# Optimization experiments

Hardware: AMD Instinct MI355X
Metric: run time of the kernel (lower is better)

Reference implementation:

```python
import jax, jax.numpy as jnp
import numpy as np

N_NODES = 50000
N_EDGES = 1600000
IN_C = 64
OUT_C = 64
N_CLASSES = 45


def setup_inputs() -> dict:
    key = jax.random.key(0)
    ks = jax.random.split(key, 12)

    def lin(k, i, o):
        return jax.random.normal(k, (i, o), jnp.float32) / np.float32(np.sqrt(i))

    return dict(
        x=jax.random.normal(ks[0], (N_NODES, IN_C), jnp.float32),
        edge_index=jax.random.randint(ks[1], (2, N_EDGES), 0, N_NODES, dtype=jnp.int32),
        W_z=lin(ks[2], IN_C, OUT_C), b_z=jnp.zeros((OUT_C,), jnp.float32),
        Wl_z=lin(ks[3], 2 * OUT_C, OUT_C), bl_z=jnp.zeros((OUT_C,), jnp.float32),
        W_r=lin(ks[4], IN_C, OUT_C), b_r=jnp.zeros((OUT_C,), jnp.float32),
        Wl_r=lin(ks[5], 2 * OUT_C, OUT_C), bl_r=jnp.zeros((OUT_C,), jnp.float32),
        W_h=lin(ks[6], IN_C, OUT_C), b_h=jnp.zeros((OUT_C,), jnp.float32),
        Wl_h=lin(ks[7], 2 * OUT_C, OUT_C), bl_h=jnp.zeros((OUT_C,), jnp.float32),
        W_out=lin(ks[8], OUT_C, N_CLASSES), b_out=jnp.zeros((N_CLASSES,), jnp.float32),
    )


def _gcn(x, W, b, src, dst, dinv):
    # GCNConv with improved self-loops (fill value 2.0):
    # out = D^{-1/2} (A + 2I) D^{-1/2} X W + b, with deg = in_degree + 2
    xw = x @ W                                   # [N, OUT_C]
    norm = dinv[src] * dinv[dst]                 # [E]
    agg = jax.ops.segment_sum(norm[:, None] * xw[src], dst, num_segments=N_NODES)
    agg = agg + (2.0 * dinv * dinv)[:, None] * xw  # self-loop contribution
    return agg + b


def reference(x, edge_index, W_z, b_z, Wl_z, bl_z, W_r, b_r, Wl_r, bl_r,
              W_h, b_h, Wl_h, bl_h, W_out, b_out):
    src, dst = edge_index[0], edge_index[1]
    deg = jax.ops.segment_sum(jnp.ones((N_EDGES,), jnp.float32), dst,
                              num_segments=N_NODES) + 2.0
    dinv = jax.lax.rsqrt(deg)

    # TGCN cell with H0 = 0 (no prior hidden state passed)
    H = jnp.zeros((N_NODES, OUT_C), x.dtype)
    Z = jax.nn.sigmoid(
        jnp.concatenate([_gcn(x, W_z, b_z, src, dst, dinv), H], axis=1) @ Wl_z + bl_z)
    R = jax.nn.sigmoid(
        jnp.concatenate([_gcn(x, W_r, b_r, src, dst, dinv), H], axis=1) @ Wl_r + bl_r)
    H_tilde = jnp.tanh(
        jnp.concatenate([_gcn(x, W_h, b_h, src, dst, dinv), H * R], axis=1) @ Wl_h + bl_h)
    H = Z * H + (1.0 - Z) * H_tilde

    # relu + linear readout to 45 classes
    return jax.nn.relu(H) @ W_out + b_out
```

## Files before the change

### kernel.cpp

```cpp
#include <hip/hip_runtime.h>

#define N_NODES 50000
#define N_EDGES 1600000
#define NB 782
#define NBB 500
#define CHUNK 3200
#define CAP 2560
#define SCAP 3072
#define ZROW 50000
#define NTILES 3125

typedef unsigned short ushort_t;
typedef _Float16 v8h __attribute__((ext_vector_type(8)));
typedef _Float16 v4h __attribute__((ext_vector_type(4)));
typedef float f32x4_t __attribute__((ext_vector_type(4)));

__global__ __launch_bounds__(256) void k_wprep2(
    const float* __restrict__ Wz, const float* __restrict__ bz,
    const float* __restrict__ Wlz, const float* __restrict__ blz,
    const float* __restrict__ Wh, const float* __restrict__ bh,
    const float* __restrict__ Wlh, const float* __restrict__ blh,
    const float* __restrict__ Wout,
    float* __restrict__ B2f, _Float16* __restrict__ Bzh,
    _Float16* __restrict__ Bwo, int* __restrict__ gcur) {
  __shared__ float A[64 * 65];
  __shared__ float Bm[64 * 65];
  int tid = threadIdx.x, blk = blockIdx.x;
  bool zpath = blk < 4;
  if (blk == 2) {
    for (int i = tid; i < NB; i += 256) gcur[i] = 0;
  }
  const float* Wsrc = zpath ? Wz : Wh;
  const float* Lsrc = zpath ? Wlz : Wlh;
  for (int idx = tid; idx < 4096; idx += 256) {
    A[(idx >> 6) * 65 + (idx & 63)] = Wsrc[idx];
    Bm[(idx >> 6) * 65 + (idx & 63)] = Lsrc[idx];
  }
  __syncthreads();

  int lane = (tid >> 1) & 63;
  int j0 = (tid & 1) * 4;
  int ks = (tid >> 7) & 1;
  int k0 = ks * 32 + ((lane >> 4) << 3) + j0;
  int col = (blk & 3) * 16 + (lane & 15);
  float a0 = 0.f, a1 = 0.f, a2 = 0.f, a3 = 0.f;
  for (int q = 0; q < 64; ++q) {
    float bv = Bm[q * 65 + col];
    a0 = fmaf(A[k0 * 65 + q], bv, a0);
    a1 = fmaf(A[(k0 + 1) * 65 + q], bv, a1);
    a2 = fmaf(A[(k0 + 2) * 65 + q], bv, a2);
    a3 = fmaf(A[(k0 + 3) * 65 + q], bv, a3);
  }
  int tb = blk * 1024 + tid * 4;
  v4h o; o[0] = (_Float16)a0; o[1] = (_Float16)a1;
  o[2] = (_Float16)a2; o[3] = (_Float16)a3;
  *(v4h*)(Bzh + tb) = o;

  if ((blk == 0 || blk == 4) && tid < 64) {
    float v = zpath ? blz[tid] : blh[tid];
    const float* bb = zpath ? bz : bh;
    for (int q = 0; q < 64; ++q) v = fmaf(bb[q], Bm[q * 65 + tid], v);
    B2f[tid * 2 + (zpath ? 0 : 1)] = v;
  }
  if (blk == 1) {
    for (int e2 = 0; e2 < 12; ++e2) {
      int t2 = tid * 12 + e2;
      int ln = (t2 >> 3) & 63, j = t2 & 7;
      int ntile = t2 >> 10, ks2 = (t2 >> 9) & 1;
      int n = ntile * 16 + (ln & 15);
      int k = ks2 * 32 + ((ln >> 4) << 3) + j;
      Bwo[t2] = (_Float16)((n < 45) ? Wout[k * 45 + n] : 0.f);
    }
  }
}

__global__ __launch_bounds__(256) void k_bin2(
    const int* __restrict__ ei, int* __restrict__ gcur, int* __restrict__ bins) {
  __shared__ int h[NB], cur[NB], segb[NB];
  __shared__ int ebuf[CHUNK];
  __shared__ int scanT[256];
  int tid = threadIdx.x, blk = blockIdx.x;
  for (int i = tid; i < NB; i += 256) h[i] = 0;
  __syncthreads();
  int e0 = blk * CHUNK;
  const int2* d2 = (const int2*)(ei + N_EDGES + e0);
  for (int i = tid; i < CHUNK / 2; i += 256) {
    int2 d = d2[i];
    atomicAdd(&h[d.x >> 6], 1);
    atomicAdd(&h[d.y >> 6], 1);
  }
  __syncthreads();
  for (int b = tid; b < NB; b += 256) {
    int c = h[b];
    segb[b] = c ? atomicAdd(&gcur[b], c) : 0;
  }
  int vals[4], ts = 0;
  #pragma unroll
  for (int r = 0; r < 4; ++r) {
    int idx = tid * 4 + r;
    int v = (idx < NB) ? h[idx] : 0;
    vals[r] = v; ts += v;
  }
  scanT[tid] = ts;
  __syncthreads();
  for (int off = 1; off < 256; off <<= 1) {
    int u = (tid >= off) ? scanT[tid - off] : 0;
    __syncthreads();
    scanT[tid] += u;
    __syncthreads();
  }
  int ex = scanT[tid] - ts;
  #pragma unroll
  for (int r = 0; r < 4; ++r) {
    int idx = tid * 4 + r;
    if (idx < NB) cur[idx] = ex;
    ex += vals[r];
  }
  __syncthreads();
  const int2* s2 = (const int2*)(ei + e0);
  for (int i = tid; i < CHUNK / 2; i += 256) {
    int2 s = s2[i];
    int2 d = d2[i];
    int b0 = d.x >> 6, b1 = d.y >> 6;
    int p0 = atomicAdd(&cur[b0], 1);
    ebuf[p0] = s.x | ((d.x & 63) << 16) | (b0 << 22);
    int p1 = atomicAdd(&cur[b1], 1);
    ebuf[p1] = s.y | ((d.y & 63) << 16) | (b1 << 22);
  }
  __syncthreads();
  for (int i = tid; i < CHUNK; i += 256) {
    int v = ebuf[i];
    int b = (unsigned)v >> 22;
    int ex0 = cur[b] - h[b];
    bins[b * CAP + segb[b] + (i - ex0)] = v & 0x3FFFFF;
  }
}

__global__ __launch_bounds__(256, 4) void k_sort(
    const int* __restrict__ bins, const int* __restrict__ gcur,
    const float* __restrict__ x,
    ushort_t* __restrict__ srcp, int2* __restrict__ rowiv,
    float* __restrict__ dinv, _Float16* __restrict__ xp) {
  __shared__ int dg[64], lo[64], cur[64];
  __shared__ float sdin[64];
  __shared__ int Tsh;
  __shared__ ushort_t buf[3072];
  int tid = threadIdx.x, b = blockIdx.x;
  int start = b * CAP, end = start + gcur[b];
  if (tid < 64) dg[tid] = 0;
  __syncthreads();
  for (int i = start + tid; i < end; i += 256)
    atomicAdd(&dg[bins[i] >> 16], 1);
  __syncthreads();
  int pdv = 0;
  if (tid < 64) { pdv = (dg[tid] + 7) & ~7; lo[tid] = pdv; }
  __syncthreads();
  for (int off = 1; off < 64; off <<= 1) {
    int u = 0;
    if (tid < 64 && tid >= off) u = lo[tid - off];
    __syncthreads();
    if (tid < 64) lo[tid] += u;
    __syncthreads();
  }
  int ex = 0;
  if (tid < 64) {
    ex = lo[tid] - pdv;
    cur[tid] = ex;
    if (tid == 63) Tsh = lo[63];
  }
  __syncthreads();
  int T = Tsh;
  int base = b * SCAP;
  for (int i = tid; i < T; i += 256) buf[i] = (ushort_t)ZROW;
  __syncthreads();
  for (int i = start + tid; i < end; i += 256) {
    int v = bins[i];
    int dl = v >> 16;
    int p = atomicAdd(&cur[dl], 1);
    buf[p] = (ushort_t)(v & 0xFFFF);
  }
  __syncthreads();
  for (int i = tid; i < T; i += 256) srcp[base + i] = buf[i];
  if (tid < 64) {
    int v = b * 64 + tid;
    if (v < N_NODES) {
      rowiv[v] = make_int2(base + ex, pdv);
      float dv = rsqrtf((float)dg[tid] + 2.0f);
      dinv[v] = dv;
      sdin[tid] = dv;
    } else {
      sdin[tid] = 0.f;
    }
  }
  __syncthreads();
  int nb64 = b * 4096;
  for (int idx = tid; idx < 4096; idx += 256) {
    int v = b * 64 + (idx >> 6);
    if (v < N_NODES) xp[nb64 + idx] = (_Float16)(sdin[idx >> 6] * x[nb64 + idx]);
  }
  if (b == 0 && tid < 64) xp[ZROW * 64 + tid] = (_Float16)0.f;
}

__global__ __launch_bounds__(256) void k_agg(
    const ushort_t* __restrict__ srcp, const int2* __restrict__ rowiv,
    const float* __restrict__ dinv, const _Float16* __restrict__ xp,
    _Float16* __restrict__ sxg) {
  int tid = threadIdx.x;
  int lane = tid & 63;
  int grp = lane >> 4;
  int sub = lane & 15;
  int chOff = sub << 2;
  int w = blockIdx.x * 4 + (tid >> 6);
  int nw = gridDim.x * 4;
  for (int v = w; v < N_NODES; v += nw) {
    int vu = __builtin_amdgcn_readfirstlane(v);
    int2 ri = rowiv[vu];
    int beg = ri.x, pd = ri.y;
    float aA0 = 0.f, aA1 = 0.f, aA2 = 0.f, aA3 = 0.f;
    float aB0 = 0.f, aB1 = 0.f, aB2 = 0.f, aB3 = 0.f;
    float aC0 = 0.f, aC1 = 0.f, aC2 = 0.f, aC3 = 0.f;
    float aD0 = 0.f, aD1 = 0.f, aD2 = 0.f, aD3 = 0.f;
    for (int e = beg; e < beg + pd; e += 64) {
      int rem = beg + pd - e;
      int m = rem < 64 ? rem : 64;
      int sv = (lane < m) ? (int)srcp[e + lane] : ZROW;
      int t = 0;
      for (; t + 16 <= m; t += 16) {
        int sA = __builtin_amdgcn_ds_bpermute((t + grp) << 2, sv);
        int sB = __builtin_amdgcn_ds_bpermute((t + 4 + grp) << 2, sv);
        int sC = __builtin_amdgcn_ds_bpermute((t + 8 + grp) << 2, sv);
        int sD = __builtin_amdgcn_ds_bpermute((t + 12 + grp) << 2, sv);
        v4h rA = *(const v4h*)(xp + (sA << 6) + chOff);
        v4h rB = *(const v4h*)(xp + (sB << 6) + chOff);
        v4h rC = *(const v4h*)(xp + (sC << 6) + chOff);
        v4h rD = *(const v4h*)(xp + (sD << 6) + chOff);
        aA0 += (float)rA[0]; aA1 += (float)rA[1];
        aA2 += (float)rA[2]; aA3 += (float)rA[3];
        aB0 += (float)rB[0]; aB1 += (float)rB[1];
        aB2 += (float)rB[2]; aB3 += (float)rB[3];
        aC0 += (float)rC[0]; aC1 += (float)rC[1];
        aC2 += (float)rC[2]; aC3 += (float)rC[3];
        aD0 += (float)rD[0]; aD1 += (float)rD[1];
        aD2 += (float)rD[2]; aD3 += (float)rD[3];
      }
      if (t < m) {
        int sA = __builtin_amdgcn_ds_bpermute((t + grp) << 2, sv);
        int sB = __builtin_amdgcn_ds_bpermute((t + 4 + grp) << 2, sv);
        v4h rA = *(const v4h*)(xp + (sA << 6) + chOff);
        v4h rB = *(const v4h*)(xp + (sB << 6) + chOff);
        aA0 += (float)rA[0]; aA1 += (float)rA[1];
        aA2 += (float)rA[2]; aA3 += (float)rA[3];
        aB0 += (float)rB[0]; aB1 += (float)rB[1];
        aB2 += (float)rB[2]; aB3 += (float)rB[3];
      }
    }
    float a0 = (aA0 + aB0) + (aC0 + aD0);
    float a1 = (aA1 + aB1) + (aC1 + aD1);
    float a2 = (aA2 + aB2) + (aC2 + aD2);
    float a3 = (aA3 + aB3) + (aC3 + aD3);
    a0 += __shfl_xor(a0, 16); a1 += __shfl_xor(a1, 16);
    a2 += __shfl_xor(a2, 16); a3 += __shfl_xor(a3, 16);
    a0 += __shfl_xor(a0, 32); a1 += __shfl_xor(a1, 32);
    a2 += __shfl_xor(a2, 32); a3 += __shfl_xor(a3, 32);
    if (lane < 16) {
      float dv = dinv[vu];
      v4h self = *(const v4h*)(xp + (vu << 6) + chOff);
      v4h o;
      o[0] = (_Float16)(dv * a0 + 2.f * dv * (float)self[0]);
      o[1] = (_Float16)(dv * a1 + 2.f * dv * (float)self[1]);
      o[2] = (_Float16)(dv * a2 + 2.f * dv * (float)self[2]);
      o[3] = (_Float16)(dv * a3 + 2.f * dv * (float)self[3]);
      *(v4h*)(sxg + (vu << 6) + chOff) = o;
    }
  }
}

__global__ __launch_bounds__(256) void k_cell(
    const _Float16* __restrict__ sxg, const _Float16* __restrict__ Bzh,
    const _Float16* __restrict__ Bwo, const float2* __restrict__ B2,
    const float* __restrict__ bout, float* __restrict__ out) {
  __shared__ __align__(16) _Float16 tbuf[4][16][72];
  int tid = threadIdx.x;
  int lane = tid & 63, wv = tid >> 6;
  int l15 = lane & 15, quad = lane >> 4;
  int tile = blockIdx.x * 4 + wv;
  if (tile >= NTILES) return;

  v8h bzf[8][2], bwf[3][2];
  #pragma unroll
  for (int t = 0; t < 8; ++t)
    #pragma unroll
    for (int ks = 0; ks < 2; ++ks)
      bzf[t][ks] = *(const v8h*)(Bzh + (((t * 2 + ks) * 64 + lane) << 3));
  #pragma unroll
  for (int t = 0; t < 3; ++t)
    #pragma unroll
    for (int ks = 0; ks < 2; ++ks)
      bwf[t][ks] = *(const v8h*)(Bwo + (((t * 2 + ks) * 64 + lane) << 3));
  float zb[4], hb[4], ob[3];
  #pragma unroll
  for (int t = 0; t < 4; ++t) {
    float2 bb = B2[t * 16 + l15];
    zb[t] = bb.x; hb[t] = bb.y;
  }
  #pragma unroll
  for (int t = 0; t < 3; ++t) {
    int c = t * 16 + l15;
    ob[t] = (c < 45) ? bout[c] : 0.f;
  }

  const _Float16* ar = sxg + (tile * 16 + l15) * 64 + quad * 8;
  v8h a0 = *(const v8h*)ar;
  v8h a1 = *(const v8h*)(ar + 32);

  f32x4_t accz[8];
  #pragma unroll
  for (int t = 0; t < 8; ++t) {
    f32x4_t c4 = {0.f, 0.f, 0.f, 0.f};
    c4 = __builtin_amdgcn_mfma_f32_16x16x32_f16(a0, bzf[t][0], c4, 0, 0, 0);
    c4 = __builtin_amdgcn_mfma_f32_16x16x32_f16(a1, bzf[t][1], c4, 0, 0, 0);
    accz[t] = c4;
  }

  #pragma unroll
  for (int t = 0; t < 4; ++t) {
    #pragma unroll
    for (int r = 0; r < 4; ++r) {
      float zv = accz[t][r] + zb[t];
      float hv = accz[t + 4][r] + hb[t];
      float Z = 1.f / (1.f + __expf(-zv));
      float tt = fminf(15.f, fmaxf(-15.f, hv));
      float e2 = __expf(-2.f * tt);
      float Th = (1.f - e2) / (1.f + e2);
      tbuf[wv][quad * 4 + r][t * 16 + l15] = (_Float16)fmaxf((1.f - Z) * Th, 0.f);
    }
  }
  __asm__ volatile("s_waitcnt lgkmcnt(0)" ::: "memory");

  v8h p0 = *(const v8h*)&tbuf[wv][l15][quad * 8];
  v8h p1 = *(const v8h*)&tbuf[wv][l15][32 + quad * 8];

  #pragma unroll
  for (int t = 0; t < 3; ++t) {
    f32x4_t o4 = {0.f, 0.f, 0.f, 0.f};
    o4 = __builtin_amdgcn_mfma_f32_16x16x32_f16(p0, bwf[t][0], o4, 0, 0, 0);
    o4 = __builtin_amdgcn_mfma_f32_16x16x32_f16(p1, bwf[t][1], o4, 0, 0, 0);
    int c = t * 16 + l15;
    if (c < 45) {
      #pragma unroll
      for (int r = 0; r < 4; ++r)
        out[(tile * 16 + quad * 4 + r) * 45 + c] = o4[r] + ob[t];
    }
  }
}

extern "C" void kernel_launch(void* const* d_in, const int* in_sizes, int n_in,
                              void* d_out, int out_size, void* d_ws, size_t ws_size,
                              hipStream_t stream) {
  const float* x    = (const float*)d_in[0];
  const int*   ei   = (const int*)d_in[1];
  const float* Wz   = (const float*)d_in[2];
  const float* bz   = (const float*)d_in[3];
  const float* Wlz  = (const float*)d_in[4];
  const float* blz  = (const float*)d_in[5];
  const float* Wh   = (const float*)d_in[10];
  const float* bh   = (const float*)d_in[11];
  const float* Wlh  = (const float*)d_in[12];
  const float* blh  = (const float*)d_in[13];
  const float* Wout = (const float*)d_in[14];
  const float* bout = (const float*)d_in[15];
  float* out = (float*)d_out;

  char* w = (char*)d_ws;
  int*      bins  = (int*)(w + 0);
  _Float16* sxg   = (_Float16*)(w + 0);
  int*      gcur  = (int*)(w + 8007680);
  ushort_t* srcp  = (ushort_t*)(w + 8010816);
  int2*     rowiv = (int2*)(w + 12815424);
  float*    dinv  = (float*)(w + 13215424);
  float2*   B2    = (float2*)(w + 13415424);
  _Float16* Bzh   = (_Float16*)(w + 13415936);
  _Float16* Bwo   = (_Float16*)(w + 13432320);
  _Float16* xp    = (_Float16*)(w + 13438464);

  k_wprep2<<<8, 256, 0, stream>>>(Wz, bz, Wlz, blz, Wh, bh, Wlh, blh, Wout,
                                  (float*)B2, Bzh, Bwo, gcur);
  k_bin2 <<<NBB, 256, 0, stream>>>(ei, gcur, bins);
  k_sort <<<NB, 256, 0, stream>>>(bins, gcur, x, srcp, rowiv, dinv, xp);
  k_agg  <<<2048, 256, 0, stream>>>(srcp, rowiv, dinv, xp, sxg);
  k_cell <<<NB, 256, 0, stream>>>(sxg, Bzh, Bwo, B2, bout, out);
}
```

Baseline: 171.9 us.

## Fuse aggregation into cell kernel and merge weight prep with edge binning

The GCN aggregation is merged into the MFMA cell kernel. Each wave aggregates its 16-node tile into shared memory instead of writing sxg to global memory and reading it back. Weight preprocessing is folded into the binning kernel as extra blocks, and gcur is now zeroed by a memset. Binning uses larger chunks and a simpler per-bin local counter instead of a prefix-scan compaction. Risks: lower parallelism in aggregation (one wave per 16 consecutive nodes, 782 blocks), less coalesced bin writes, and a possibly insufficient LDS sync using only waitcnt within a wave.

```diff
diff --git a/kernel.cpp b/kernel.cpp
--- a/kernel.cpp
+++ b/kernel.cpp
@@ -3,8 +3,8 @@
 #define N_NODES 50000
 #define N_EDGES 1600000
 #define NB 782
-#define NBB 500
-#define CHUNK 3200
+#define NBB 256
+#define CHUNK 6250
 #define CAP 2560
 #define SCAP 3072
 #define ZROW 50000
@@ -15,124 +15,97 @@
 typedef _Float16 v4h __attribute__((ext_vector_type(4)));
 typedef float f32x4_t __attribute__((ext_vector_type(4)));
 
-__global__ __launch_bounds__(256) void k_wprep2(
+__device__ __forceinline__ int rlanei(int v, int l) {
+  return __builtin_amdgcn_readlane(v, l);
+}
+__device__ __forceinline__ float rlanef(float v, int l) {
+  return __int_as_float(__builtin_amdgcn_readlane(__float_as_int(v), l));
+}
+
+__global__ __launch_bounds__(256) void k_binw(
+    const int* __restrict__ ei, int* __restrict__ gcur, int* __restrict__ bins,
     const float* __restrict__ Wz, const float* __restrict__ bz,
     const float* __restrict__ Wlz, const float* __restrict__ blz,
     const float* __restrict__ Wh, const float* __restrict__ bh,
     const float* __restrict__ Wlh, const float* __restrict__ blh,
-    const float* __restrict__ Wout,
-    float* __restrict__ B2f, _Float16* __restrict__ Bzh,
-    _Float16* __restrict__ Bwo, int* __restrict__ gcur) {
-  __shared__ float A[64 * 65];
-  __shared__ float Bm[64 * 65];
+    const float* __restrict__ Wout, float* __restrict__ B2f,
+    _Float16* __restrict__ Bzh, _Float16* __restrict__ Bwo) {
+  __shared__ int arena[8320];
   int tid = threadIdx.x, blk = blockIdx.x;
-  bool zpath = blk < 4;
-  if (blk == 2) {
-    for (int i = tid; i < NB; i += 256) gcur[i] = 0;
-  }
-  const float* Wsrc = zpath ? Wz : Wh;
-  const float* Lsrc = zpath ? Wlz : Wlh;
-  for (int idx = tid; idx < 4096; idx += 256) {
-    A[(idx >> 6) * 65 + (idx & 63)] = Wsrc[idx];
-    Bm[(idx >> 6) * 65 + (idx & 63)] = Lsrc[idx];
-  }
-  __syncthreads();
-
-  int lane = (tid >> 1) & 63;
-  int j0 = (tid & 1) * 4;
-  int ks = (tid >> 7) & 1;
-  int k0 = ks * 32 + ((lane >> 4) << 3) + j0;
-  int col = (blk & 3) * 16 + (lane & 15);
-  float a0 = 0.f, a1 = 0.f, a2 = 0.f, a3 = 0.f;
-  for (int q = 0; q < 64; ++q) {
-    float bv = Bm[q * 65 + col];
-    a0 = fmaf(A[k0 * 65 + q], bv, a0);
-    a1 = fmaf(A[(k0 + 1) * 65 + q], bv, a1);
-    a2 = fmaf(A[(k0 + 2) * 65 + q], bv, a2);
-    a3 = fmaf(A[(k0 + 3) * 65 + q], bv, a3);
-  }
-  int tb = blk * 1024 + tid * 4;
-  v4h o; o[0] = (_Float16)a0; o[1] = (_Float16)a1;
-  o[2] = (_Float16)a2; o[3] = (_Float16)a3;
-  *(v4h*)(Bzh + tb) = o;
-
-  if ((blk == 0 || blk == 4) && tid < 64) {
-    float v = zpath ? blz[tid] : blh[tid];
-    const float* bb = zpath ? bz : bh;
-    for (int q = 0; q < 64; ++q) v = fmaf(bb[q], Bm[q * 65 + tid], v);
-    B2f[tid * 2 + (zpath ? 0 : 1)] = v;
-  }
-  if (blk == 1) {
-    for (int e2 = 0; e2 < 12; ++e2) {
-      int t2 = tid * 12 + e2;
-      int ln = (t2 >> 3) & 63, j = t2 & 7;
-      int ntile = t2 >> 10, ks2 = (t2 >> 9) & 1;
-      int n = ntile * 16 + (ln & 15);
-      int k = ks2 * 32 + ((ln >> 4) << 3) + j;
-      Bwo[t2] = (_Float16)((n < 45) ? Wout[k * 45 + n] : 0.f);
-    }
-  }
-}
-
-__global__ __launch_bounds__(256) void k_bin2(
-    const int* __restrict__ ei, int* __restrict__ gcur, int* __restrict__ bins) {
-  __shared__ int h[NB], cur[NB], segb[NB];
-  __shared__ int ebuf[CHUNK];
-  __shared__ int scanT[256];
-  int tid = threadIdx.x, blk = blockIdx.x;
-  for (int i = tid; i < NB; i += 256) h[i] = 0;
-  __syncthreads();
-  int e0 = blk * CHUNK;
-  const int2* d2 = (const int2*)(ei + N_EDGES + e0);
-  for (int i = tid; i < CHUNK / 2; i += 256) {
-    int2 d = d2[i];
-    atomicAdd(&h[d.x >> 6], 1);
-    atomicAdd(&h[d.y >> 6], 1);
-  }
-  __syncthreads();
-  for (int b = tid; b < NB; b += 256) {
-    int c = h[b];
-    segb[b] = c ? atomicAdd(&gcur[b], c) : 0;
-  }
-  int vals[4], ts = 0;
-  #pragma unroll
-  for (int r = 0; r < 4; ++r) {
-    int idx = tid * 4 + r;
-    int v = (idx < NB) ? h[idx] : 0;
-    vals[r] = v; ts += v;
-  }
-  scanT[tid] = ts;
-  __syncthreads();
-  for (int off = 1; off < 256; off <<= 1) {
-    int u = (tid >= off) ? scanT[tid - off] : 0;
-    __syncthreads();
-    scanT[tid] += u;
-    __syncthreads();
-  }
-  int ex = scanT[tid] - ts;
-  #pragma unroll
-  for (int r = 0; r < 4; ++r) {
-    int idx = tid * 4 + r;
-    if (idx < NB) cur[idx] = ex;
-    ex += vals[r];
-  }
-  __syncthreads();
-  const int2* s2 = (const int2*)(ei + e0);
-  for (int i = tid; i < CHUNK / 2; i += 256) {
-    int2 s = s2[i];
-    int2 d = d2[i];
-    int b0 = d.x >> 6, b1 = d.y >> 6;
-    int p0 = atomicAdd(&cur[b0], 1);
-    ebuf[p0] = s.x | ((d.x & 63) << 16) | (b0 << 22);
-    int p1 = atomicAdd(&cur[b1], 1);
-    ebuf[p1] = s.y | ((d.y & 63) << 16) | (b1 << 22);
-  }
-  __syncthreads();
-  for (int i = tid; i < CHUNK; i += 256) {
-    int v = ebuf[i];
-    int b = (unsigned)v >> 22;
-    int ex0 = cur[b] - h[b];
-    bins[b * CAP + segb[b] + (i - ex0)] = v & 0x3FFFFF;
+  if (blk < NBB) {
+    int* h    = arena;
+    int* segb = arena + NB;
+    int* pk   = arena + 2 * NB;
+    for (int i = tid; i < NB; i += 256) h[i] = 0;
+    __syncthreads();
+    const int2* s2 = (const int2*)(ei + blk * CHUNK);
+    const int2* d2 = (const int2*)(ei + N_EDGES + blk * CHUNK);
+    for (int i = tid; i < CHUNK / 2; i += 256) {
+      int2 s = s2[i];
+      int2 d = d2[i];
+      pk[2 * i]     = s.x | ((d.x & 63) << 16) | ((d.x >> 6) << 22);
+      pk[2 * i + 1] = s.y | ((d.y & 63) << 16) | ((d.y >> 6) << 22);
+      atomicAdd(&h[d.x >> 6], 1);
+      atomicAdd(&h[d.y >> 6], 1);
+    }
+    __syncthreads();
+    for (int b = tid; b < NB; b += 256) {
+      int c = h[b];
+      segb[b] = c ? atomicAdd(&gcur[b], c) : 0;
+      h[b] = 0;
+    }
+    __syncthreads();
+    for (int i = tid; i < CHUNK; i += 256) {
+      int v = pk[i];
+      int b = (unsigned)v >> 22;
+      int p = atomicAdd(&h[b], 1);
+      bins[b * CAP + segb[b] + p] = v & 0x3FFFFF;
+    }
+  } else {
+    int wblk = blk - NBB;
+    float* A  = (float*)arena;
+    float* Bm = (float*)(arena + 4160);
+    bool zpath = wblk < 4;
+    const float* Wsrc = zpath ? Wz : Wh;
+    const float* Lsrc = zpath ? Wlz : Wlh;
+    for (int idx = tid; idx < 4096; idx += 256) {
+      A[(idx >> 6) * 65 + (idx & 63)] = Wsrc[idx];
+      Bm[(idx >> 6) * 65 + (idx & 63)] = Lsrc[idx];
+    }
+    __syncthreads();
+    int lane = (tid >> 1) & 63;
+    int j0 = (tid & 1) * 4;
+    int ks = (tid >> 7) & 1;
+    int k0 = ks * 32 + ((lane >> 4) << 3) + j0;
+    int col = (wblk & 3) * 16 + (lane & 15);
+    float a0 = 0.f, a1 = 0.f, a2 = 0.f, a3 = 0.f;
+    for (int q = 0; q < 64; ++q) {
+      float bv = Bm[q * 65 + col];
+      a0 = fmaf(A[k0 * 65 + q], bv, a0);
+      a1 = fmaf(A[(k0 + 1) * 65 + q], bv, a1);
+      a2 = fmaf(A[(k0 + 2) * 65 + q], bv, a2);
+      a3 = fmaf(A[(k0 + 3) * 65 + q], bv, a3);
+    }
+    int tb = wblk * 1024 + tid * 4;
+    v4h o; o[0] = (_Float16)a0; o[1] = (_Float16)a1;
+    o[2] = (_Float16)a2; o[3] = (_Float16)a3;
+    *(v4h*)(Bzh + tb) = o;
+    if ((wblk == 0 || wblk == 4) && tid < 64) {
+      float v = zpath ? blz[tid] : blh[tid];
+      const float* bb = zpath ? bz : bh;
+      for (int q = 0; q < 64; ++q) v = fmaf(bb[q], Bm[q * 65 + tid], v);
+      B2f[tid * 2 + (zpath ? 0 : 1)] = v;
+    }
+    if (wblk == 1) {
+      for (int e2 = 0; e2 < 12; ++e2) {
+        int t2 = tid * 12 + e2;
+        int ln = (t2 >> 3) & 63, j = t2 & 7;
+        int ntile = t2 >> 10, ks2 = (t2 >> 9) & 1;
+        int n = ntile * 16 + (ln & 15);
+        int k = ks2 * 32 + ((ln >> 4) << 3) + j;
+        Bwo[t2] = (_Float16)((n < 45) ? Wout[k * 45 + n] : 0.f);
+      }
+    }
   }
 }
 
@@ -201,35 +174,42 @@
   if (b == 0 && tid < 64) xp[ZROW * 64 + tid] = (_Float16)0.f;
 }
 
-__global__ __launch_bounds__(256) void k_agg(
+__global__ __launch_bounds__(256) void k_gcell(
     const ushort_t* __restrict__ srcp, const int2* __restrict__ rowiv,
     const float* __restrict__ dinv, const _Float16* __restrict__ xp,
-    _Float16* __restrict__ sxg) {
+    const _Float16* __restrict__ Bzh, const _Float16* __restrict__ Bwo,
+    const float2* __restrict__ B2, const float* __restrict__ bout,
+    float* __restrict__ out) {
+  __shared__ __align__(16) _Float16 tbuf[4][16][72];
   int tid = threadIdx.x;
-  int lane = tid & 63;
-  int grp = lane >> 4;
-  int sub = lane & 15;
-  int chOff = sub << 2;
-  int w = blockIdx.x * 4 + (tid >> 6);
-  int nw = gridDim.x * 4;
-  for (int v = w; v < N_NODES; v += nw) {
-    int vu = __builtin_amdgcn_readfirstlane(v);
-    int2 ri = rowiv[vu];
-    int beg = ri.x, pd = ri.y;
-    float aA0 = 0.f, aA1 = 0.f, aA2 = 0.f, aA3 = 0.f;
-    float aB0 = 0.f, aB1 = 0.f, aB2 = 0.f, aB3 = 0.f;
-    float aC0 = 0.f, aC1 = 0.f, aC2 = 0.f, aC3 = 0.f;
-    float aD0 = 0.f, aD1 = 0.f, aD2 = 0.f, aD3 = 0.f;
+  int lane = tid & 63, wv = tid >> 6;
+  int tile = blockIdx.x * 4 + wv;
+  if (tile >= NTILES) return;
+  int l15 = lane & 15, quad = lane >> 4;
+  int chOff = l15 << 2;
+
+  int rbx = 0, rby = 0; float dvv = 0.f;
+  if (lane < 16) {
+    int2 ri = rowiv[tile * 16 + lane];
+    rbx = ri.x; rby = ri.y;
+    dvv = dinv[tile * 16 + lane];
+  }
+
+  for (int n = 0; n < 16; ++n) {
+    int beg = rlanei(rbx, n);
+    int pd  = rlanei(rby, n);
+    float aA0=0.f,aA1=0.f,aA2=0.f,aA3=0.f, aB0=0.f,aB1=0.f,aB2=0.f,aB3=0.f;
+    float aC0=0.f,aC1=0.f,aC2=0.f,aC3=0.f, aD0=0.f,aD1=0.f,aD2=0.f,aD3=0.f;
     for (int e = beg; e < beg + pd; e += 64) {
       int rem = beg + pd - e;
       int m = rem < 64 ? rem : 64;
       int sv = (lane < m) ? (int)srcp[e + lane] : ZROW;
       int t = 0;
       for (; t + 16 <= m; t += 16) {
-        int sA = __builtin_amdgcn_ds_bpermute((t + grp) << 2, sv);
-        int sB = __builtin_amdgcn_ds_bpermute((t + 4 + grp) << 2, sv);
-        int sC = __builtin_amdgcn_ds_bpermute((t + 8 + grp) << 2, sv);
-        int sD = __builtin_amdgcn_ds_bpermute((t + 12 + grp) << 2, sv);
+        int sA = __builtin_amdgcn_ds_bpermute((t + quad) << 2, sv);
+        int sB = __builtin_amdgcn_ds_bpermute((t + 4 + quad) << 2, sv);
+        int sC = __builtin_amdgcn_ds_bpermute((t + 8 + quad) << 2, sv);
+        int sD = __builtin_amdgcn_ds_bpermute((t + 12 + quad) << 2, sv);
         v4h rA = *(const v4h*)(xp + (sA << 6) + chOff);
         v4h rB = *(const v4h*)(xp + (sB << 6) + chOff);
         v4h rC = *(const v4h*)(xp + (sC << 6) + chOff);
@@ -244,8 +224,8 @@
         aD2 += (float)rD[2]; aD3 += (float)rD[3];
       }
       if (t < m) {
-        int sA = __builtin_amdgcn_ds_bpermute((t + grp) << 2, sv);
-        int sB = __builtin_amdgcn_ds_bpermute((t + 4 + grp) << 2, sv);
+        int sA = __builtin_amdgcn_ds_bpermute((t + quad) << 2, sv);
+        int sB = __builtin_amdgcn_ds_bpermute((t + 4 + quad) << 2, sv);
         v4h rA = *(const v4h*)(xp + (sA << 6) + chOff);
         v4h rB = *(const v4h*)(xp + (sB << 6) + chOff);
         aA0 += (float)rA[0]; aA1 += (float)rA[1];
@@ -263,28 +243,20 @@
     a0 += __shfl_xor(a0, 32); a1 += __shfl_xor(a1, 32);
     a2 += __shfl_xor(a2, 32); a3 += __shfl_xor(a3, 32);
     if (lane < 16) {
-      float dv = dinv[vu];
-      v4h self = *(const v4h*)(xp + (vu << 6) + chOff);
+      float dv = rlanef(dvv, n);
+      v4h self = *(const v4h*)(xp + ((tile * 16 + n) << 6) + chOff);
       v4h o;
       o[0] = (_Float16)(dv * a0 + 2.f * dv * (float)self[0]);
       o[1] = (_Float16)(dv * a1 + 2.f * dv * (float)self[1]);
       o[2] = (_Float16)(dv * a2 + 2.f * dv * (float)self[2]);
       o[3] = (_Float16)(dv * a3 + 2.f * dv * (float)self[3]);
-      *(v4h*)(sxg + (vu << 6) + chOff) = o;
-    }
-  }
-}
-
-__global__ __launch_bounds__(256) void k_cell(
-    const _Float16* __restrict__ sxg, const _Float16* __restrict__ Bzh,
-    const _Float16* __restrict__ Bwo, const float2* __restrict__ B2,
-    const float* __restrict__ bout, float* __restrict__ out) {
-  __shared__ __align__(16) _Float16 tbuf[4][16][72];
-  int tid = threadIdx.x;
-  int lane = tid & 63, wv = tid >> 6;
-  int l15 = lane & 15, quad = lane >> 4;
-  int tile = blockIdx.x * 4 + wv;
-  if (tile >= NTILES) return;
+      *(v4h*)&tbuf[wv][n][chOff] = o;
+    }
+  }
+  __asm__ volatile("s_waitcnt lgkmcnt(0)" ::: "memory");
+
+  v8h a0 = *(const v8h*)&tbuf[wv][l15][quad * 8];
+  v8h a1 = *(const v8h*)&tbuf[wv][l15][32 + quad * 8];
 
   v8h bzf[8][2], bwf[3][2];
   #pragma unroll
@@ -308,10 +280,6 @@
     int c = t * 16 + l15;
     ob[t] = (c < 45) ? bout[c] : 0.f;
   }
-
-  const _Float16* ar = sxg + (tile * 16 + l15) * 64 + quad * 8;
-  v8h a0 = *(const v8h*)ar;
-  v8h a1 = *(const v8h*)(ar + 32);
 
   f32x4_t accz[8];
   #pragma unroll
@@ -373,7 +341,6 @@
 
   char* w = (char*)d_ws;
   int*      bins  = (int*)(w + 0);
-  _Float16* sxg   = (_Float16*)(w + 0);
   int*      gcur  = (int*)(w + 8007680);
   ushort_t* srcp  = (ushort_t*)(w + 8010816);
   int2*     rowiv = (int2*)(w + 12815424);
@@ -383,10 +350,11 @@
   _Float16* Bwo   = (_Float16*)(w + 13432320);
   _Float16* xp    = (_Float16*)(w + 13438464);
 
-  k_wprep2<<<8, 256, 0, stream>>>(Wz, bz, Wlz, blz, Wh, bh, Wlh, blh, Wout,
-                                  (float*)B2, Bzh, Bwo, gcur);
-  k_bin2 <<<NBB, 256, 0, stream>>>(ei, gcur, bins);
+  hipMemsetAsync(gcur, 0, NB * sizeof(int), stream);
+  k_binw <<<NBB + 8, 256, 0, stream>>>(ei, gcur, bins, Wz, bz, Wlz, blz,
+                                       Wh, bh, Wlh, blh, Wout,
+                                       (float*)B2, Bzh, Bwo);
   k_sort <<<NB, 256, 0, stream>>>(bins, gcur, x, srcp, rowiv, dinv, xp);
-  k_agg  <<<2048, 256, 0, stream>>>(srcp, rowiv, dinv, xp, sxg);
-  k_cell <<<NB, 256, 0, stream>>>(sxg, Bzh, Bwo, B2, bout, out);
-}
+  k_gcell<<<NB, 256, 0, stream>>>(srcp, rowiv, dinv, xp, Bzh, Bwo, B2,
+                                  bout, out);
+}
```

Measured after the change: 174.3 us. Within noise of the previous version (+1.4%).

## Simplify edge binning: drop local scan, scatter with LDS atomics, larger chunks

Applied to the files above, without the earlier changes.

The binning kernel no longer builds a block-local exclusive scan and reorders edges in shared memory. It packs edges into LDS on the first pass, then scatters each edge straight to its global bin slot using an LDS atomic counter per bin. Chunk size grows so fewer blocks are launched, which means fewer global atomics on bin counters. The trade-off is less coalesced global writes, because edges are no longer grouped by bin before the scatter. The sort kernel's shared buffer is enlarged as well, which may lower occupancy.

```diff
diff --git a/kernel.cpp b/kernel.cpp
--- a/kernel.cpp
+++ b/kernel.cpp
@@ -3,8 +3,8 @@
 #define N_NODES 50000
 #define N_EDGES 1600000
 #define NB 782
-#define NBB 500
-#define CHUNK 3200
+#define NBB 256
+#define CHUNK 6250
 #define CAP 2560
 #define SCAP 3072
 #define ZROW 50000
@@ -76,16 +76,19 @@
 
 __global__ __launch_bounds__(256) void k_bin2(
     const int* __restrict__ ei, int* __restrict__ gcur, int* __restrict__ bins) {
-  __shared__ int h[NB], cur[NB], segb[NB];
-  __shared__ int ebuf[CHUNK];
-  __shared__ int scanT[256];
+  __shared__ int h[NB];
+  __shared__ int segb[NB];
+  __shared__ int pk[CHUNK];
   int tid = threadIdx.x, blk = blockIdx.x;
   for (int i = tid; i < NB; i += 256) h[i] = 0;
   __syncthreads();
-  int e0 = blk * CHUNK;
-  const int2* d2 = (const int2*)(ei + N_EDGES + e0);
+  const int2* s2 = (const int2*)(ei + blk * CHUNK);
+  const int2* d2 = (const int2*)(ei + N_EDGES + blk * CHUNK);
   for (int i = tid; i < CHUNK / 2; i += 256) {
+    int2 s = s2[i];
     int2 d = d2[i];
+    pk[2 * i]     = s.x | ((d.x & 63) << 16) | ((d.x >> 6) << 22);
+    pk[2 * i + 1] = s.y | ((d.y & 63) << 16) | ((d.y >> 6) << 22);
     atomicAdd(&h[d.x >> 6], 1);
     atomicAdd(&h[d.y >> 6], 1);
   }
@@ -93,46 +96,14 @@
   for (int b = tid; b < NB; b += 256) {
     int c = h[b];
     segb[b] = c ? atomicAdd(&gcur[b], c) : 0;
-  }
-  int vals[4], ts = 0;
-  #pragma unroll
-  for (int r = 0; r < 4; ++r) {
-    int idx = tid * 4 + r;
-    int v = (idx < NB) ? h[idx] : 0;
-    vals[r] = v; ts += v;
-  }
-  scanT[tid] = ts;
-  __syncthreads();
-  for (int off = 1; off < 256; off <<= 1) {
-    int u = (tid >= off) ? scanT[tid - off] : 0;
-    __syncthreads();
-    scanT[tid] += u;
-    __syncthreads();
-  }
-  int ex = scanT[tid] - ts;
-  #pragma unroll
-  for (int r = 0; r < 4; ++r) {
-    int idx = tid * 4 + r;
-    if (idx < NB) cur[idx] = ex;
-    ex += vals[r];
-  }
-  __syncthreads();
-  const int2* s2 = (const int2*)(ei + e0);
-  for (int i = tid; i < CHUNK / 2; i += 256) {
-    int2 s = s2[i];
-    int2 d = d2[i];
-    int b0 = d.x >> 6, b1 = d.y >> 6;
-    int p0 = atomicAdd(&cur[b0], 1);
-    ebuf[p0] = s.x | ((d.x & 63) << 16) | (b0 << 22);
-    int p1 = atomicAdd(&cur[b1], 1);
-    ebuf[p1] = s.y | ((d.y & 63) << 16) | (b1 << 22);
+    h[b] = 0;
   }
   __syncthreads();
   for (int i = tid; i < CHUNK; i += 256) {
-    int v = ebuf[i];
+    int v = pk[i];
     int b = (unsigned)v >> 22;
-    int ex0 = cur[b] - h[b];
-    bins[b * CAP + segb[b] + (i - ex0)] = v & 0x3FFFFF;
+    int p = atomicAdd(&h[b], 1);
+    bins[b * CAP + segb[b] + p] = v & 0x3FFFFF;
   }
 }
 
@@ -144,7 +115,7 @@
   __shared__ int dg[64], lo[64], cur[64];
   __shared__ float sdin[64];
   __shared__ int Tsh;
-  __shared__ ushort_t buf[3072];
+  __shared__ ushort_t buf[8192];
   int tid = threadIdx.x, b = blockIdx.x;
   int start = b * CAP, end = start + gcur[b];
   if (tid < 64) dg[tid] = 0;
@@ -216,10 +187,8 @@
     int vu = __builtin_amdgcn_readfirstlane(v);
     int2 ri = rowiv[vu];
     int beg = ri.x, pd = ri.y;
-    float aA0 = 0.f, aA1 = 0.f, aA2 = 0.f, aA3 = 0.f;
-    float aB0 = 0.f, aB1 = 0.f, aB2 = 0.f, aB3 = 0.f;
-    float aC0 = 0.f, aC1 = 0.f, aC2 = 0.f, aC3 = 0.f;
-    float aD0 = 0.f, aD1 = 0.f, aD2 = 0.f, aD3 = 0.f;
+    float aA0=0.f,aA1=0.f,aA2=0.f,aA3=0.f, aB0=0.f,aB1=0.f,aB2=0.f,aB3=0.f;
+    float aC0=0.f,aC1=0.f,aC2=0.f,aC3=0.f, aD0=0.f,aD1=0.f,aD2=0.f,aD3=0.f;
     for (int e = beg; e < beg + pd; e += 64) {
       int rem = beg + pd - e;
       int m = rem < 64 ? rem : 64;
```

After: 165.2 us. 1.04x faster.
